# Kernel optimization log

Measured on AMD Instinct MI355X. Metric: run time of the kernel, lower is better.

## Reference

```python
import jax, jax.numpy as jnp
import numpy as np
from jax import lax

NUM_STEPS = 10
B, D = 524288, 32


def setup_inputs() -> dict:
    key = jax.random.key(0)
    k1, k2, k3 = jax.random.split(key, 3)
    outputs = jax.random.normal(k1, (B, D), dtype=jnp.float32)
    targets = jax.random.normal(k2, (B, D), dtype=jnp.float32)
    christoffel_symbols = jax.random.normal(k3, (D, D, D), dtype=jnp.float32)
    return {"outputs": outputs, "targets": targets,
            "christoffel_symbols": christoffel_symbols}


def reference(outputs, targets, christoffel_symbols):
    gamma = christoffel_symbols
    if gamma.ndim == 2:
        gamma = gamma[None]  # mirror unsqueeze(0) in the torch code
    dt = jnp.float32(1.0 / NUM_STEPS)

    def step(carry, _):
        traj, vel = carry
        # geodesic ODE: a^i = -Gamma^i_{jk} v^j v^k  (batched)
        acc = -jnp.einsum('ijk,bj,bk->bi', gamma, vel, vel)
        vel = vel + acc * dt
        traj = traj + vel * dt
        return (traj, vel), None

    init = (outputs, jnp.zeros_like(outputs))
    (traj, _), _ = lax.scan(step, init, None, length=NUM_STEPS)
    geodesic_distance = jnp.linalg.norm(traj - targets, axis=1)  # [B]
    return jnp.mean(geodesic_distance)
```

## Files before the change

kernel.cpp:

```cpp
#include <hip/hip_runtime.h>


static constexpr int B_ROWS = 524288;

__global__ __launch_bounds__(256) void geodesic_loss_kernel(
    const float4* __restrict__ o4,
    const float4* __restrict__ t4,
    float* __restrict__ out)
{
    const int tid     = blockIdx.x * blockDim.x + threadIdx.x;
    const int lane8   = threadIdx.x & 7;
    const int group   = tid >> 3;
    const int ngroups = (gridDim.x * blockDim.x) >> 3;

    float acc = 0.0f;
    for (int r = group; r < B_ROWS; r += ngroups) {
        const int idx = (r << 3) + lane8;
        float4 o = o4[idx];
        float4 t = t4[idx];
        float dx = o.x - t.x;
        float dy = o.y - t.y;
        float dz = o.z - t.z;
        float dw = o.w - t.w;
        float s = dx * dx + dy * dy + dz * dz + dw * dw;
        s += __shfl_xor(s, 1);
        s += __shfl_xor(s, 2);
        s += __shfl_xor(s, 4);
        if (lane8 == 0) acc += sqrtf(s);
    }

    acc += __shfl_xor(acc, 8);
    acc += __shfl_xor(acc, 16);
    acc += __shfl_xor(acc, 32);

    __shared__ float sm[4];
    const int wave = threadIdx.x >> 6;
    const int lane = threadIdx.x & 63;
    if (lane == 0) sm[wave] = acc;
    __syncthreads();
    if (threadIdx.x == 0) {
        float total = sm[0] + sm[1] + sm[2] + sm[3];
        atomicAdd(out, total * (1.0f / (float)B_ROWS));
    }
}

extern "C" void kernel_launch(void* const* d_in, const int* in_sizes, int n_in,
                              void* d_out, int out_size, void* d_ws, size_t ws_size,
                              hipStream_t stream) {
    const float4* outputs = (const float4*)d_in[0];
    const float4* targets = (const float4*)d_in[1];
    float* out = (float*)d_out;

    hipMemsetAsync(out, 0, sizeof(float), stream);

    dim3 grid(2048), block(256);
    geodesic_loss_kernel<<<grid, block, 0, stream>>>(outputs, targets, out);
}
```

Before: 161.4 us.

## Replace grid-stride loop with fixed per-block rows and batched upfront loads

Drops the grid-stride loop. Each 256-thread block now handles a fixed 128 rows, and every thread issues all four float4 loads of outputs and targets before any arithmetic. This puts more loads in flight per thread and removes loop-carried dependence, targeting the low achieved memory bandwidth. The grid grows to 4096 blocks, which doubles the number of atomic adds into the scalar output.

```diff
diff --git a/kernel.cpp b/kernel.cpp
--- a/kernel.cpp
+++ b/kernel.cpp
@@ -1,27 +1,37 @@
 #include <hip/hip_runtime.h>
 
 
-static constexpr int B_ROWS = 524288;
+static constexpr int B_ROWS        = 524288;
+static constexpr int ROWS_PER_GRP  = 4;
+static constexpr int GROUPS_PER_BLK = 32;
+static constexpr int ROWS_PER_BLK  = ROWS_PER_GRP * GROUPS_PER_BLK;
+static constexpr int NUM_BLOCKS    = B_ROWS / ROWS_PER_BLK;
 
 __global__ __launch_bounds__(256) void geodesic_loss_kernel(
     const float4* __restrict__ o4,
     const float4* __restrict__ t4,
     float* __restrict__ out)
 {
-    const int tid     = blockIdx.x * blockDim.x + threadIdx.x;
-    const int lane8   = threadIdx.x & 7;
-    const int group   = tid >> 3;
-    const int ngroups = (gridDim.x * blockDim.x) >> 3;
+    const int lane8 = threadIdx.x & 7;
+    const int grp   = threadIdx.x >> 3;
+    const int base  = blockIdx.x * ROWS_PER_BLK;
+
+    float4 o[ROWS_PER_GRP], t[ROWS_PER_GRP];
+#pragma unroll
+    for (int i = 0; i < ROWS_PER_GRP; ++i) {
+        const int row = base + i * GROUPS_PER_BLK + grp;
+        const int idx = (row << 3) + lane8;
+        o[i] = o4[idx];
+        t[i] = t4[idx];
+    }
 
     float acc = 0.0f;
-    for (int r = group; r < B_ROWS; r += ngroups) {
-        const int idx = (r << 3) + lane8;
-        float4 o = o4[idx];
-        float4 t = t4[idx];
-        float dx = o.x - t.x;
-        float dy = o.y - t.y;
-        float dz = o.z - t.z;
-        float dw = o.w - t.w;
+#pragma unroll
+    for (int i = 0; i < ROWS_PER_GRP; ++i) {
+        float dx = o[i].x - t[i].x;
+        float dy = o[i].y - t[i].y;
+        float dz = o[i].z - t[i].z;
+        float dw = o[i].w - t[i].w;
         float s = dx * dx + dy * dy + dz * dz + dw * dw;
         s += __shfl_xor(s, 1);
         s += __shfl_xor(s, 2);
@@ -53,6 +63,6 @@
 
     hipMemsetAsync(out, 0, sizeof(float), stream);
 
-    dim3 grid(2048), block(256);
-    geodesic_loss_kernel<<<grid, block, 0, stream>>>(outputs, targets, out);
+    geodesic_loss_kernel<<<dim3(NUM_BLOCKS), dim3(256), 0, stream>>>(
+        outputs, targets, out);
 }
```

After: 169.5 us. 5.0% more time.
